# Performance work log

Measured on AMD Instinct MI355X. Metric: run time of the kernel, lower is better.

The kernel has to match this reference:

```python
import math
import jax, jax.numpy as jnp
import numpy as np

B, S, T, C, H = 4, 100, 128, 256, 256
NH, DH = 4, 32            # num_attention_heads//2, hidden_size//num_attention_heads
AH = NH * DH              # all_head_size = 128
FH = 32                   # fire_hidden_size
MAX_SP, MAX_TM, MAX_DOY = 180.0, 365.0, 182.0


def _fire(dist, c, w1, w2, max_dist):
    # FIREDistanceBias: log-compressed distance -> MLP(1->FH, SiLU, FH->1, no bias)
    c = jnp.maximum(c, 0.0)
    d = jnp.log(c * dist + 1.0) / jnp.log(c * max_dist + 1.0)
    h = jax.nn.silu(d[..., None] * w1[:, 0])   # (..., FH)
    return h @ w2[0]                            # (...,)


def setup_inputs() -> dict:
    key = jax.random.key(0)
    ks = jax.random.split(key, 20)
    p = 0.02
    inp = {
        "hidden_states": jax.random.normal(ks[0], (B, S, T, H), jnp.float32),
        "source_embeddings": jax.random.normal(ks[1], (B, S, C, H), jnp.float32),
        "attention_mask": jnp.zeros((B, 1, 1, T, C), jnp.float32),
        "st_dist": jax.random.uniform(ks[2], (B, T, C, 2), jnp.float32)
                   * jnp.array([MAX_SP, MAX_TM], jnp.float32),
        "st_doy_dist": jax.random.uniform(ks[3], (B, T, C), jnp.float32) * MAX_DOY,
        # attention projections (Linear H->AH with bias), output dense (AH->H)
        "Wq": jax.random.normal(ks[4], (AH, H), jnp.float32) * p,
        "bq": jnp.zeros((AH,), jnp.float32),
        "Wk": jax.random.normal(ks[5], (AH, H), jnp.float32) * p,
        "bk": jnp.zeros((AH,), jnp.float32),
        "Wv": jax.random.normal(ks[6], (AH, H), jnp.float32) * p,
        "bv": jnp.zeros((AH,), jnp.float32),
        "Wo": jax.random.normal(ks[7], (H, AH), jnp.float32) * p,
        "bo": jnp.zeros((H,), jnp.float32),
        # FIRE params: spatial / temporal / seasonal
        "c_s": jnp.float32(100.0),
        "w1_s": jax.random.normal(ks[8], (FH, 1), jnp.float32) * 0.5,
        "w2_s": jax.random.normal(ks[9], (1, FH), jnp.float32) * 0.5,
        "c_t": jnp.float32(100.0),
        "w1_t": jax.random.normal(ks[10], (FH, 1), jnp.float32) * 0.5,
        "w2_t": jax.random.normal(ks[11], (1, FH), jnp.float32) * 0.5,
        "c_d": jnp.float32(100.0),
        "w1_d": jax.random.normal(ks[12], (FH, 1), jnp.float32) * 0.5,
        "w2_d": jax.random.normal(ks[13], (1, FH), jnp.float32) * 0.5,
        # per-species log scales (init zeros in torch)
        "s_log_scale": jnp.zeros((S,), jnp.float32),
        "t_log_scale": jnp.zeros((S,), jnp.float32),
    }
    return inp


def reference(hidden_states, source_embeddings, attention_mask, st_dist, st_doy_dist,
              Wq, bq, Wk, bk, Wv, bv, Wo, bo,
              c_s, w1_s, w2_s, c_t, w1_t, w2_t, c_d, w1_d, w2_d,
              s_log_scale, t_log_scale):
    # FIRE distance biases over (B, T, C)
    sb = _fire(st_dist[..., 0], c_s, w1_s, w2_s, MAX_SP)
    tb = _fire(st_dist[..., 1], c_t, w1_t, w2_t, MAX_TM)
    db = _fire(st_doy_dist, c_d, w1_d, w2_d, MAX_DOY)
    # (B, S, T, C): species-scaled spatial+temporal + seasonal bias
    bias = (sb[:, None] * jnp.exp(s_log_scale)[None, :, None, None]
            + tb[:, None] * jnp.exp(t_log_scale)[None, :, None, None]
            + db[:, None])

    # projections; split heads: (B,S,L,AH) -> (B,S,NH,L,DH)
    q = (hidden_states @ Wq.T + bq).reshape(B, S, T, NH, DH).transpose(0, 1, 3, 2, 4)
    k = (source_embeddings @ Wk.T + bk).reshape(B, S, C, NH, DH).transpose(0, 1, 3, 2, 4)
    v = (source_embeddings @ Wv.T + bv).reshape(B, S, C, NH, DH).transpose(0, 1, 3, 2, 4)

    scores = jnp.einsum('bshtd,bshcd->bshtc', q, k) / math.sqrt(DH)
    scores = scores + attention_mask + bias[:, :, None]   # mask (B,1,1,T,C), bias (B,S,1,T,C)
    probs = jax.nn.softmax(scores, axis=-1)
    ctx = jnp.einsum('bshtc,bshcd->bshtd', probs, v)
    ctx = ctx.transpose(0, 1, 3, 2, 4).reshape(B, S, T, AH)
    return ctx @ Wo.T + bo   # STCrossOutput dense (dropout=0, eval)
```

## Files before the change

### kernel.cpp

```cpp
#include <hip/hip_runtime.h>
#include <hip/hip_bf16.h>
#include <math.h>

#define Bdim 4
#define Sdim 100
#define Tdim 128
#define Cdim 256
#define Hdim 256
#define NHd  4
#define DHd  32
#define AHd  128

typedef short bf16x8 __attribute__((ext_vector_type(8)));
typedef float f32x4 __attribute__((ext_vector_type(4)));

#define WAITCNT_V(n) do { \
  asm volatile("s_waitcnt vmcnt(" #n ")" ::: "memory"); \
  __builtin_amdgcn_sched_barrier(0); \
} while (0)

__device__ __forceinline__ short f2b(float x) {
  unsigned u = __float_as_uint(x);
  unsigned r = (u + 0x7FFF + ((u >> 16) & 1)) >> 16;
  return (short)r;
}

__device__ __forceinline__ void split2(float x, short& hi, short& lo) {
  unsigned u = __float_as_uint(x) & 0xFFFF0000u;
  hi = (short)(u >> 16);
  lo = f2b(x - __uint_as_float(u));
}

__device__ __forceinline__ float fire_eval(float dist, float c,
                                           const float* __restrict__ w1,
                                           const float* __restrict__ w2,
                                           float maxd) {
  c = fmaxf(c, 0.0f);
  float d = logf(fmaf(c, dist, 1.0f)) / logf(fmaf(c, maxd, 1.0f));
  float acc = 0.0f;
#pragma unroll
  for (int j = 0; j < 32; ++j) {
    float x = d * w1[j];
    float h = x / (1.0f + expf(-x));
    acc = fmaf(h, w2[j], acc);
  }
  return acc;
}

__global__ __launch_bounds__(256) void fire_bias_kernel(
    const float* __restrict__ st_dist, const float* __restrict__ st_doy,
    const float* __restrict__ mask,
    const float* __restrict__ c_s, const float* __restrict__ w1_s, const float* __restrict__ w2_s,
    const float* __restrict__ c_t, const float* __restrict__ w1_t, const float* __restrict__ w2_t,
    const float* __restrict__ c_d, const float* __restrict__ w1_d, const float* __restrict__ w2_d,
    float4* __restrict__ pk) {
  int i = blockIdx.x * 256 + threadIdx.x;
  if (i >= Bdim * Tdim * Cdim) return;
  float2 dv = ((const float2*)st_dist)[i];
  float4 r;
  r.x = fire_eval(dv.x, c_s[0], w1_s, w2_s, 180.0f);
  r.y = fire_eval(dv.y, c_t[0], w1_t, w2_t, 365.0f);
  r.z = fire_eval(st_doy[i], c_d[0], w1_d, w2_d, 182.0f) + mask[i];
  r.w = 0.0f;
  pk[i] = r;
}

__global__ __launch_bounds__(256) void bias_combine(
    const float4* __restrict__ pk,
    const float* __restrict__ sls, const float* __restrict__ tls,
    float* __restrict__ bC) {
  const int b = blockIdx.y;
  const int base = blockIdx.x * 1024 + threadIdx.x * 4;
  const float4* src = pk + (size_t)b * Tdim * Cdim + base;
  float sb[4], tb[4], db[4];
#pragma unroll
  for (int i = 0; i < 4; ++i) {
    float4 v = src[i];
    sb[i] = v.x; tb[i] = v.y; db[i] = v.z;
  }
  float* dst = bC + ((size_t)b * Sdim) * Tdim * Cdim + base;
  for (int s = 0; s < Sdim; ++s) {
    float es = __expf(sls[s]), et = __expf(tls[s]);
    float4 o;
    o.x = fmaf(sb[0], es, fmaf(tb[0], et, db[0]));
    o.y = fmaf(sb[1], es, fmaf(tb[1], et, db[1]));
    o.z = fmaf(sb[2], es, fmaf(tb[2], et, db[2]));
    o.w = fmaf(sb[3], es, fmaf(tb[3], et, db[3]));
    *(float4*)(dst + (size_t)s * Tdim * Cdim) = o;
  }
}

__global__ __launch_bounds__(256) void wsplit_pack(
    const float* __restrict__ Wq, const float* __restrict__ Wk,
    const float* __restrict__ Wv, const float* __restrict__ Wo,
    short* __restrict__ pack) {
  int which = blockIdx.y;
  const float* W = which == 0 ? Wq : which == 1 ? Wk : which == 2 ? Wv : Wo;
  int idx = blockIdx.x * 256 + threadIdx.x;
  int j = idx & 7;
  int l = (idx >> 3) & 63;
  int frag = idx >> 9;
  int nt, kk8, Kd;
  if (which == 3) { nt = frag & 15; kk8 = frag >> 4; Kd = 128; }
  else           { nt = frag & 7;  kk8 = frag >> 3; Kd = 256; }
  int n = nt * 16 + (l & 15);
  int k = kk8 * 32 + (l >> 4) * 8 + j;
  short h, lo_;
  split2(W[(size_t)n * Kd + k], h, lo_);
  pack[(size_t)which * 65536 + idx] = h;
  pack[(size_t)which * 65536 + 32768 + idx] = lo_;
}


__global__ __launch_bounds__(512, 4) void proj_q_mfma(
    const float* __restrict__ A, const short* __restrict__ Wp,
    const float* __restrict__ bias, short* __restrict__ O, float scale) {
  __shared__ short wlds[2][16 * 512];
  const int tid = threadIdx.x;
  const int l = tid & 63, w = tid >> 6;
  const int lr = l & 15, lg = l >> 4;
  const int m0 = blockIdx.x * 128;
  const int arow = m0 + w * 16 + lr;
  const float* ap = A + (size_t)arow * 256 + lg * 8;

  auto stage = [&](int buf, int kk) {
#pragma unroll
    for (int r = 0; r < 2; ++r) {
      int f = w + 8 * r;
      const short* gsrc = Wp + (r ? 32768 : 0) + ((size_t)(kk * 8 + w) * 64 + l) * 8;
      int loff = __builtin_amdgcn_readfirstlane(buf * 8192 + f * 512);
      __builtin_amdgcn_global_load_lds(gsrc, &wlds[0][0] + loff, 16, 0, 0);
    }
  };

  f32x4 acc[8] = {};
  stage(0, 0);
  float4 ca = *(const float4*)ap;
  float4 cb = *(const float4*)(ap + 4);
#pragma unroll
  for (int kk = 0; kk < 8; ++kk) {
    const int buf = kk & 1;
    float4 na, nb;
    if (kk < 7) {
      stage(buf ^ 1, kk + 1);
      const float* np = ap + (kk + 1) * 32;
      na = *(const float4*)np;
      nb = *(const float4*)(np + 4);
    }
    float av[8] = {ca.x, ca.y, ca.z, ca.w, cb.x, cb.y, cb.z, cb.w};
    bf16x8 ahi, alo;
#pragma unroll
    for (int e = 0; e < 8; ++e) { short h, lo_; split2(av[e], h, lo_); ahi[e] = h; alo[e] = lo_; }
    if (kk < 7) { WAITCNT_V(4); } else { WAITCNT_V(0); }
    __builtin_amdgcn_s_barrier();
    const short* lb = &wlds[0][0] + buf * 8192 + l * 8;
#pragma unroll
    for (int nt = 0; nt < 8; ++nt) {
      bf16x8 whi = *(const bf16x8*)(lb + nt * 512);
      bf16x8 wlo = *(const bf16x8*)(lb + (8 + nt) * 512);
      acc[nt] = __builtin_amdgcn_mfma_f32_16x16x32_bf16(ahi, whi, acc[nt], 0, 0, 0);
      acc[nt] = __builtin_amdgcn_mfma_f32_16x16x32_bf16(ahi, wlo, acc[nt], 0, 0, 0);
      acc[nt] = __builtin_amdgcn_mfma_f32_16x16x32_bf16(alo, whi, acc[nt], 0, 0, 0);
    }
    __builtin_amdgcn_s_barrier();
    if (kk < 7) { ca = na; cb = nb; }
  }
#pragma unroll
  for (int nt = 0; nt < 8; ++nt)
#pragma unroll
    for (int r = 0; r < 4; ++r)
      O[(size_t)(m0 + w * 16 + lg * 4 + r) * 128 + nt * 16 + lr] =
          f2b((acc[nt][r] + bias[nt * 16 + lr]) * scale);
}

__global__ __launch_bounds__(512, 4) void proj_kv_mfma(
    const float* __restrict__ A,
    const short* __restrict__ Wkp, const float* __restrict__ bk,
    const short* __restrict__ Wvp, const float* __restrict__ bv,
    short* __restrict__ Ko, short* __restrict__ Vo) {
  __shared__ short wlds[2][32 * 512];
  const int tid = threadIdx.x;
  const int l = tid & 63, w = tid >> 6;
  const int lr = l & 15, lg = l >> 4;
  const int m0 = blockIdx.x * 128;
  const int arow = m0 + w * 16 + lr;
  const float* ap = A + (size_t)arow * 256 + lg * 8;

  auto stage = [&](int buf, int kk) {
#pragma unroll
    for (int r = 0; r < 4; ++r) {
      int f = w + 8 * r;
      const short* gsrc = ((f >> 4) ? Wvp : Wkp) + (((f >> 3) & 1) ? 32768 : 0)
                          + ((size_t)(kk * 8 + (f & 7)) * 64 + l) * 8;
      int loff = __builtin_amdgcn_readfirstlane(buf * 16384 + f * 512);
      __builtin_amdgcn_global_load_lds(gsrc, &wlds[0][0] + loff, 16, 0, 0);
    }
  };

  f32x4 accK[8] = {}, accV[8] = {};
  stage(0, 0);
  float4 ca = *(const float4*)ap;
  float4 cb = *(const float4*)(ap + 4);
#pragma unroll
  for (int kk = 0; kk < 8; ++kk) {
    const int buf = kk & 1;
    float4 na, nb;
    if (kk < 7) {
      stage(buf ^ 1, kk + 1);
      const float* np = ap + (kk + 1) * 32;
      na = *(const float4*)np;
      nb = *(const float4*)(np + 4);
    }
    float av[8] = {ca.x, ca.y, ca.z, ca.w, cb.x, cb.y, cb.z, cb.w};
    bf16x8 ahi, alo;
#pragma unroll
    for (int e = 0; e < 8; ++e) { short h, lo_; split2(av[e], h, lo_); ahi[e] = h; alo[e] = lo_; }
    if (kk < 7) { WAITCNT_V(6); } else { WAITCNT_V(0); }
    __builtin_amdgcn_s_barrier();
    const short* lb = &wlds[0][0] + buf * 16384 + l * 8;
#pragma unroll
    for (int nt = 0; nt < 8; ++nt) {
      bf16x8 khi = *(const bf16x8*)(lb + nt * 512);
      bf16x8 klo = *(const bf16x8*)(lb + (8 + nt) * 512);
      bf16x8 vhi = *(const bf16x8*)(lb + (16 + nt) * 512);
      bf16x8 vlo = *(const bf16x8*)(lb + (24 + nt) * 512);
      accK[nt] = __builtin_amdgcn_mfma_f32_16x16x32_bf16(ahi, khi, accK[nt], 0, 0, 0);
      accK[nt] = __builtin_amdgcn_mfma_f32_16x16x32_bf16(ahi, klo, accK[nt], 0, 0, 0);
      accK[nt] = __builtin_amdgcn_mfma_f32_16x16x32_bf16(alo, khi, accK[nt], 0, 0, 0);
      accV[nt] = __builtin_amdgcn_mfma_f32_16x16x32_bf16(ahi, vhi, accV[nt], 0, 0, 0);
      accV[nt] = __builtin_amdgcn_mfma_f32_16x16x32_bf16(ahi, vlo, accV[nt], 0, 0, 0);
      accV[nt] = __builtin_amdgcn_mfma_f32_16x16x32_bf16(alo, vhi, accV[nt], 0, 0, 0);
    }
    __builtin_amdgcn_s_barrier();
    if (kk < 7) { ca = na; cb = nb; }
  }
#pragma unroll
  for (int nt = 0; nt < 8; ++nt)
#pragma unroll
    for (int r = 0; r < 4; ++r) {
      size_t row = (size_t)(m0 + w * 16 + lg * 4 + r) * 128 + nt * 16 + lr;
      Ko[row] = f2b(accK[nt][r] + bk[nt * 16 + lr]);
      Vo[row] = f2b(accV[nt][r] + bv[nt * 16 + lr]);
    }
}

__global__ __launch_bounds__(512, 4) void proj_o_mfma(
    const short* __restrict__ Ahi, const short* __restrict__ Alo,
    const short* __restrict__ Wp, const float* __restrict__ bias,
    float* __restrict__ O) {
  __shared__ short wlds[2][32 * 512];
  const int tid = threadIdx.x;
  const int l = tid & 63, w = tid >> 6;
  const int lr = l & 15, lg = l >> 4;
  const int m0 = blockIdx.x * 128;
  const int arow = m0 + w * 16 + lr;
  const short* ah = Ahi + (size_t)arow * 128 + lg * 8;
  const short* al = Alo + (size_t)arow * 128 + lg * 8;

  auto stage = [&](int buf, int kk) {
#pragma unroll
    for (int r = 0; r < 4; ++r) {
      int f = w + 8 * r;
      const short* gsrc = Wp + ((f >> 4) ? 32768 : 0)
                          + ((size_t)(kk * 16 + (f & 15)) * 64 + l) * 8;
      int loff = __builtin_amdgcn_readfirstlane(buf * 16384 + f * 512);
      __builtin_amdgcn_global_load_lds(gsrc, &wlds[0][0] + loff, 16, 0, 0);
    }
  };

  f32x4 acc[16] = {};
  stage(0, 0);
  bf16x8 cah = *(const bf16x8*)ah;
  bf16x8 cal = *(const bf16x8*)al;
#pragma unroll
  for (int kk = 0; kk < 4; ++kk) {
    const int buf = kk & 1;
    bf16x8 nah, nal;
    if (kk < 3) {
      stage(buf ^ 1, kk + 1);
      nah = *(const bf16x8*)(ah + (kk + 1) * 32);
      nal = *(const bf16x8*)(al + (kk + 1) * 32);
    }
    if (kk < 3) { WAITCNT_V(6); } else { WAITCNT_V(0); }
    __builtin_amdgcn_s_barrier();
    const short* lb = &wlds[0][0] + buf * 16384 + l * 8;
#pragma unroll
    for (int nt = 0; nt < 16; ++nt) {
      bf16x8 whi = *(const bf16x8*)(lb + nt * 512);
      bf16x8 wlo = *(const bf16x8*)(lb + (16 + nt) * 512);
      acc[nt] = __builtin_amdgcn_mfma_f32_16x16x32_bf16(cah, whi, acc[nt], 0, 0, 0);
      acc[nt] = __builtin_amdgcn_mfma_f32_16x16x32_bf16(cah, wlo, acc[nt], 0, 0, 0);
      acc[nt] = __builtin_amdgcn_mfma_f32_16x16x32_bf16(cal, whi, acc[nt], 0, 0, 0);
    }
    __builtin_amdgcn_s_barrier();
    if (kk < 3) { cah = nah; cal = nal; }
  }
#pragma unroll
  for (int nt = 0; nt < 16; ++nt)
#pragma unroll
    for (int r = 0; r < 4; ++r)
      O[(size_t)(m0 + w * 16 + lg * 4 + r) * 256 + nt * 16 + lr] =
          acc[nt][r] + bias[nt * 16 + lr];
}

__global__ __launch_bounds__(512) void attn_mfma(
    const short* __restrict__ Qb, const short* __restrict__ Kb,
    const short* __restrict__ Vb,
    const float* __restrict__ bC,
    short* __restrict__ Chi, short* __restrict__ Clo) {
  __shared__ short vfrag[8][2][64][8];
  __shared__ short pbuf[8][16 * 36];

  const int tid = threadIdx.x;
  const int l = tid & 63;
  const int w = tid >> 6;
  const int lr = l & 15, lg = l >> 4;
  const int bid = blockIdx.x;
  const int xcd = bid & 7;
  const int i_  = bid >> 3;
  const int bs  = xcd * 50 + (i_ >> 2);
  const int h   = i_ & 3;

  const size_t kvbase = (size_t)bs * Cdim * AHd + h * DHd;
  const size_t qbase  = (size_t)bs * Tdim * AHd + h * DHd;

#pragma unroll
  for (int rep = 0; rep < 2; ++rep) {
    int chunk = tid * 2 + rep;
    int c = chunk >> 2, q = chunk & 3;
    bf16x8 v8 = *(const bf16x8*)(Vb + kvbase + (size_t)c * AHd + q * 8);
    int kc = c >> 5, nt = q >> 1;
    int lanebase = ((c & 31) >> 3) * 16 + (q & 1) * 8;
    int j = c & 7;
#pragma unroll
    for (int e = 0; e < 8; ++e)
      vfrag[kc][nt][lanebase + e][j] = v8[e];
  }
  __syncthreads();

  bf16x8 qf = *(const bf16x8*)(Qb + qbase + (size_t)(w * 16 + lr) * AHd + lg * 8);
  bf16x8 kf[16];
#pragma unroll
  for (int nt = 0; nt < 16; ++nt)
    kf[nt] = *(const bf16x8*)(Kb + kvbase + (size_t)(nt * 16 + lr) * AHd + lg * 8);

  const float* bb = bC + (size_t)bs * Tdim * Cdim + (size_t)(w * 16) * Cdim;
  f32x4 sacc[16];
#pragma unroll
  for (int nt = 0; nt < 16; ++nt) {
    f32x4 cinit;
#pragma unroll
    for (int r = 0; r < 4; ++r)
      cinit[r] = bb[(size_t)(lg * 4 + r) * Cdim + nt * 16 + lr];
    sacc[nt] = __builtin_amdgcn_mfma_f32_16x16x32_bf16(qf, kf[nt], cinit, 0, 0, 0);
  }

  float rinv[4];
#pragma unroll
  for (int nt = 0; nt < 16; ++nt)
#pragma unroll
    for (int r = 0; r < 4; ++r)
      sacc[nt][r] = __expf(sacc[nt][r]);
#pragma unroll
  for (int r = 0; r < 4; ++r) {
    float su = 0.f;
#pragma unroll
    for (int nt = 0; nt < 16; ++nt) su += sacc[nt][r];
#pragma unroll
    for (int off = 1; off < 16; off <<= 1) su += __shfl_xor(su, off);
    rinv[r] = 1.0f / su;
  }

  const f32x4 zero = {0.f, 0.f, 0.f, 0.f};
  f32x4 cacc[2] = {zero, zero};
  short* pb = &pbuf[w][0];
#pragma unroll
  for (int kc = 0; kc < 8; ++kc) {
#pragma unroll
    for (int ntl = 0; ntl < 2; ++ntl) {
      int nt = kc * 2 + ntl;
#pragma unroll
      for (int r = 0; r < 4; ++r)
        pb[(lg * 4 + r) * 36 + ntl * 16 + lr] = f2b(sacc[nt][r]);
    }
    bf16x8 af = *(const bf16x8*)&pb[lr * 36 + lg * 8];
#pragma unroll
    for (int ntd = 0; ntd < 2; ++ntd) {
      bf16x8 vf = *(const bf16x8*)&vfrag[kc][ntd][l][0];
      cacc[ntd] = __builtin_amdgcn_mfma_f32_16x16x32_bf16(af, vf, cacc[ntd], 0, 0, 0);
    }
  }

#pragma unroll
  for (int ntd = 0; ntd < 2; ++ntd)
#pragma unroll
    for (int r = 0; r < 4; ++r) {
      float val = cacc[ntd][r] * rinv[r];
      short h_, lo_;
      split2(val, h_, lo_);
      size_t idx = qbase + (size_t)(w * 16 + lg * 4 + r) * AHd + ntd * 16 + lr;
      Chi[idx] = h_;
      Clo[idx] = lo_;
    }
}

extern "C" void kernel_launch(void* const* d_in, const int* in_sizes, int n_in,
                              void* d_out, int out_size, void* d_ws, size_t ws_size,
                              hipStream_t stream) {
  const float* hs     = (const float*)d_in[0];
  const float* se     = (const float*)d_in[1];
  const float* mask   = (const float*)d_in[2];
  const float* stdist = (const float*)d_in[3];
  const float* stdoy  = (const float*)d_in[4];
  const float* Wq = (const float*)d_in[5];
  const float* bq = (const float*)d_in[6];
  const float* Wk = (const float*)d_in[7];
  const float* bk = (const float*)d_in[8];
  const float* Wv = (const float*)d_in[9];
  const float* bv = (const float*)d_in[10];
  const float* Wo = (const float*)d_in[11];
  const float* bo = (const float*)d_in[12];
  const float* c_s  = (const float*)d_in[13];
  const float* w1_s = (const float*)d_in[14];
  const float* w2_s = (const float*)d_in[15];
  const float* c_t  = (const float*)d_in[16];
  const float* w1_t = (const float*)d_in[17];
  const float* w2_t = (const float*)d_in[18];
  const float* c_d  = (const float*)d_in[19];
  const float* w1_d = (const float*)d_in[20];
  const float* w2_d = (const float*)d_in[21];
  const float* sls  = (const float*)d_in[22];
  const float* tls  = (const float*)d_in[23];
  float* out = (float*)d_out;

  float* ws = (float*)d_ws;
  const size_t BTC  = (size_t)Bdim * Tdim * Cdim;
  const size_t BSTC = (size_t)Bdim * Sdim * Tdim * Cdim;
  const size_t NQ   = (size_t)Bdim * Sdim * Tdim * AHd;
  const size_t NKV  = (size_t)Bdim * Sdim * Cdim * AHd;

  float4* pk  = (float4*)ws;
  float* bC   = ws + 4 * BTC;
  short* wpck = (short*)(bC + BSTC);
  short* Qb   = wpck + 262144;
  short* Kb   = Qb + NQ;
  short* Vb   = Kb + NKV;
  short* Chi  = Vb + NKV;
  short* Clo  = Chi + NQ;

  const int MQ  = Bdim * Sdim * Tdim;
  const int MKV = Bdim * Sdim * Cdim;

  fire_bias_kernel<<<(Bdim * Tdim * Cdim + 255) / 256, 256, 0, stream>>>(
      stdist, stdoy, mask, c_s, w1_s, w2_s, c_t, w1_t, w2_t, c_d, w1_d, w2_d, pk);

  bias_combine<<<dim3(Tdim * Cdim / 1024, Bdim), 256, 0, stream>>>(pk, sls, tls, bC);

  wsplit_pack<<<dim3(128, 4), 256, 0, stream>>>(Wq, Wk, Wv, Wo, wpck);

  proj_q_mfma<<<dim3(MQ / 128), 512, 0, stream>>>(hs, wpck, bq, Qb,
                                                  0.17677669529663687f);
  proj_kv_mfma<<<dim3(MKV / 128), 512, 0, stream>>>(
      se, wpck + 65536, bk, wpck + 131072, bv, Kb, Vb);

  attn_mfma<<<dim3(Bdim * Sdim * NHd), 512, 0, stream>>>(
      Qb, Kb, Vb, bC, Chi, Clo);

  proj_o_mfma<<<dim3(MQ / 128), 512, 0, stream>>>(Chi, Clo, wpck + 196608, bo, out);
}
```

Before: 183.2 us.

## Retile projection GEMMs so each wave covers two M tiles and half N

The Q, KV and output projection kernels now give each wave two 16-row M tiles and half of the N columns, instead of one M tile across all N. Each LDS weight fragment read then feeds twice as many MFMAs, halving LDS read traffic per MFMA. In exchange every row of A is loaded by two waves, which doubles global/L2 reads of the activation operand and duplicates the fp32-to-bf16 split work. The wait counts are adjusted for the extra in-flight loads.

```diff
diff --git a/kernel.cpp b/kernel.cpp
--- a/kernel.cpp
+++ b/kernel.cpp
@@ -119,9 +119,10 @@
   const int tid = threadIdx.x;
   const int l = tid & 63, w = tid >> 6;
   const int lr = l & 15, lg = l >> 4;
+  const int g = w >> 2, q = w & 3;
   const int m0 = blockIdx.x * 128;
-  const int arow = m0 + w * 16 + lr;
-  const float* ap = A + (size_t)arow * 256 + lg * 8;
+  const float* ap0 = A + (size_t)(m0 + q * 32 + lr) * 256 + lg * 8;
+  const float* ap1 = ap0 + (size_t)16 * 256;
 
   auto stage = [&](int buf, int kk) {
 #pragma unroll
@@ -133,44 +134,63 @@
     }
   };
 
-  f32x4 acc[8] = {};
+  f32x4 acc[2][4] = {};
   stage(0, 0);
-  float4 ca = *(const float4*)ap;
-  float4 cb = *(const float4*)(ap + 4);
+  float4 c0a = *(const float4*)ap0;
+  float4 c0b = *(const float4*)(ap0 + 4);
+  float4 c1a = *(const float4*)ap1;
+  float4 c1b = *(const float4*)(ap1 + 4);
 #pragma unroll
   for (int kk = 0; kk < 8; ++kk) {
     const int buf = kk & 1;
-    float4 na, nb;
+    bf16x8 ahi[2], alo[2];
+    {
+      float av0[8] = {c0a.x, c0a.y, c0a.z, c0a.w, c0b.x, c0b.y, c0b.z, c0b.w};
+      float av1[8] = {c1a.x, c1a.y, c1a.z, c1a.w, c1b.x, c1b.y, c1b.z, c1b.w};
+#pragma unroll
+      for (int e = 0; e < 8; ++e) {
+        short h, lo_;
+        split2(av0[e], h, lo_); ahi[0][e] = h; alo[0][e] = lo_;
+        split2(av1[e], h, lo_); ahi[1][e] = h; alo[1][e] = lo_;
+      }
+    }
     if (kk < 7) {
       stage(buf ^ 1, kk + 1);
-      const float* np = ap + (kk + 1) * 32;
-      na = *(const float4*)np;
-      nb = *(const float4*)(np + 4);
-    }
-    float av[8] = {ca.x, ca.y, ca.z, ca.w, cb.x, cb.y, cb.z, cb.w};
-    bf16x8 ahi, alo;
-#pragma unroll
-    for (int e = 0; e < 8; ++e) { short h, lo_; split2(av[e], h, lo_); ahi[e] = h; alo[e] = lo_; }
-    if (kk < 7) { WAITCNT_V(4); } else { WAITCNT_V(0); }
+      const int nk = (kk + 1) * 32;
+      c0a = *(const float4*)(ap0 + nk);
+      c0b = *(const float4*)(ap0 + nk + 4);
+      c1a = *(const float4*)(ap1 + nk);
+      c1b = *(const float4*)(ap1 + nk + 4);
+      WAITCNT_V(6);
+    } else {
+      WAITCNT_V(0);
+    }
     __builtin_amdgcn_s_barrier();
     const short* lb = &wlds[0][0] + buf * 8192 + l * 8;
 #pragma unroll
-    for (int nt = 0; nt < 8; ++nt) {
-      bf16x8 whi = *(const bf16x8*)(lb + nt * 512);
-      bf16x8 wlo = *(const bf16x8*)(lb + (8 + nt) * 512);
-      acc[nt] = __builtin_amdgcn_mfma_f32_16x16x32_bf16(ahi, whi, acc[nt], 0, 0, 0);
-      acc[nt] = __builtin_amdgcn_mfma_f32_16x16x32_bf16(ahi, wlo, acc[nt], 0, 0, 0);
-      acc[nt] = __builtin_amdgcn_mfma_f32_16x16x32_bf16(alo, whi, acc[nt], 0, 0, 0);
+    for (int nt = 0; nt < 4; ++nt) {
+      const int ntp = g * 4 + nt;
+      bf16x8 whi = *(const bf16x8*)(lb + ntp * 512);
+      bf16x8 wlo = *(const bf16x8*)(lb + (8 + ntp) * 512);
+#pragma unroll
+      for (int mi = 0; mi < 2; ++mi) {
+        acc[mi][nt] = __builtin_amdgcn_mfma_f32_16x16x32_bf16(ahi[mi], whi, acc[mi][nt], 0, 0, 0);
+        acc[mi][nt] = __builtin_amdgcn_mfma_f32_16x16x32_bf16(ahi[mi], wlo, acc[mi][nt], 0, 0, 0);
+        acc[mi][nt] = __builtin_amdgcn_mfma_f32_16x16x32_bf16(alo[mi], whi, acc[mi][nt], 0, 0, 0);
+      }
     }
     __builtin_amdgcn_s_barrier();
-    if (kk < 7) { ca = na; cb = nb; }
-  }
-#pragma unroll
-  for (int nt = 0; nt < 8; ++nt)
-#pragma unroll
-    for (int r = 0; r < 4; ++r)
-      O[(size_t)(m0 + w * 16 + lg * 4 + r) * 128 + nt * 16 + lr] =
-          f2b((acc[nt][r] + bias[nt * 16 + lr]) * scale);
+  }
+#pragma unroll
+  for (int mi = 0; mi < 2; ++mi)
+#pragma unroll
+    for (int nt = 0; nt < 4; ++nt)
+#pragma unroll
+      for (int r = 0; r < 4; ++r) {
+        int col = (g * 4 + nt) * 16 + lr;
+        O[(size_t)(m0 + q * 32 + mi * 16 + lg * 4 + r) * 128 + col] =
+            f2b((acc[mi][nt][r] + bias[col]) * scale);
+      }
 }
 
 __global__ __launch_bounds__(512, 4) void proj_kv_mfma(
@@ -182,9 +202,10 @@
   const int tid = threadIdx.x;
   const int l = tid & 63, w = tid >> 6;
   const int lr = l & 15, lg = l >> 4;
+  const int half = w >> 2, q = w & 3;
   const int m0 = blockIdx.x * 128;
-  const int arow = m0 + w * 16 + lr;
-  const float* ap = A + (size_t)arow * 256 + lg * 8;
+  const float* ap0 = A + (size_t)(m0 + q * 32 + lr) * 256 + lg * 8;
+  const float* ap1 = ap0 + (size_t)16 * 256;
 
   auto stage = [&](int buf, int kk) {
 #pragma unroll
@@ -197,51 +218,63 @@
     }
   };
 
-  f32x4 accK[8] = {}, accV[8] = {};
+  f32x4 acc[2][8] = {};
   stage(0, 0);
-  float4 ca = *(const float4*)ap;
-  float4 cb = *(const float4*)(ap + 4);
+  float4 c0a = *(const float4*)ap0;
+  float4 c0b = *(const float4*)(ap0 + 4);
+  float4 c1a = *(const float4*)ap1;
+  float4 c1b = *(const float4*)(ap1 + 4);
 #pragma unroll
   for (int kk = 0; kk < 8; ++kk) {
     const int buf = kk & 1;
-    float4 na, nb;
+    bf16x8 ahi[2], alo[2];
+    {
+      float av0[8] = {c0a.x, c0a.y, c0a.z, c0a.w, c0b.x, c0b.y, c0b.z, c0b.w};
+      float av1[8] = {c1a.x, c1a.y, c1a.z, c1a.w, c1b.x, c1b.y, c1b.z, c1b.w};
+#pragma unroll
+      for (int e = 0; e < 8; ++e) {
+        short h, lo_;
+        split2(av0[e], h, lo_); ahi[0][e] = h; alo[0][e] = lo_;
+        split2(av1[e], h, lo_); ahi[1][e] = h; alo[1][e] = lo_;
+      }
+    }
     if (kk < 7) {
       stage(buf ^ 1, kk + 1);
-      const float* np = ap + (kk + 1) * 32;
-      na = *(const float4*)np;
-      nb = *(const float4*)(np + 4);
-    }
-    float av[8] = {ca.x, ca.y, ca.z, ca.w, cb.x, cb.y, cb.z, cb.w};
-    bf16x8 ahi, alo;
-#pragma unroll
-    for (int e = 0; e < 8; ++e) { short h, lo_; split2(av[e], h, lo_); ahi[e] = h; alo[e] = lo_; }
-    if (kk < 7) { WAITCNT_V(6); } else { WAITCNT_V(0); }
+      const int nk = (kk + 1) * 32;
+      c0a = *(const float4*)(ap0 + nk);
+      c0b = *(const float4*)(ap0 + nk + 4);
+      c1a = *(const float4*)(ap1 + nk);
+      c1b = *(const float4*)(ap1 + nk + 4);
+      WAITCNT_V(8);
+    } else {
+      WAITCNT_V(0);
+    }
     __builtin_amdgcn_s_barrier();
-    const short* lb = &wlds[0][0] + buf * 16384 + l * 8;
+    const short* lb = &wlds[0][0] + buf * 16384 + half * 16 * 512 + l * 8;
 #pragma unroll
     for (int nt = 0; nt < 8; ++nt) {
-      bf16x8 khi = *(const bf16x8*)(lb + nt * 512);
-      bf16x8 klo = *(const bf16x8*)(lb + (8 + nt) * 512);
-      bf16x8 vhi = *(const bf16x8*)(lb + (16 + nt) * 512);
-      bf16x8 vlo = *(const bf16x8*)(lb + (24 + nt) * 512);
-      accK[nt] = __builtin_amdgcn_mfma_f32_16x16x32_bf16(ahi, khi, accK[nt], 0, 0, 0);
-      accK[nt] = __builtin_amdgcn_mfma_f32_16x16x32_bf16(ahi, klo, accK[nt], 0, 0, 0);
-      accK[nt] = __builtin_amdgcn_mfma_f32_16x16x32_bf16(alo, khi, accK[nt], 0, 0, 0);
-      accV[nt] = __builtin_amdgcn_mfma_f32_16x16x32_bf16(ahi, vhi, accV[nt], 0, 0, 0);
-      accV[nt] = __builtin_amdgcn_mfma_f32_16x16x32_bf16(ahi, vlo, accV[nt], 0, 0, 0);
-      accV[nt] = __builtin_amdgcn_mfma_f32_16x16x32_bf16(alo, vhi, accV[nt], 0, 0, 0);
+      bf16x8 whi = *(const bf16x8*)(lb + nt * 512);
+      bf16x8 wlo = *(const bf16x8*)(lb + (8 + nt) * 512);
+#pragma unroll
+      for (int mi = 0; mi < 2; ++mi) {
+        acc[mi][nt] = __builtin_amdgcn_mfma_f32_16x16x32_bf16(ahi[mi], whi, acc[mi][nt], 0, 0, 0);
+        acc[mi][nt] = __builtin_amdgcn_mfma_f32_16x16x32_bf16(ahi[mi], wlo, acc[mi][nt], 0, 0, 0);
+        acc[mi][nt] = __builtin_amdgcn_mfma_f32_16x16x32_bf16(alo[mi], whi, acc[mi][nt], 0, 0, 0);
+      }
     }
     __builtin_amdgcn_s_barrier();
-    if (kk < 7) { ca = na; cb = nb; }
-  }
-#pragma unroll
-  for (int nt = 0; nt < 8; ++nt)
-#pragma unroll
-    for (int r = 0; r < 4; ++r) {
-      size_t row = (size_t)(m0 + w * 16 + lg * 4 + r) * 128 + nt * 16 + lr;
-      Ko[row] = f2b(accK[nt][r] + bk[nt * 16 + lr]);
-      Vo[row] = f2b(accV[nt][r] + bv[nt * 16 + lr]);
-    }
+  }
+  short* __restrict__ O = half ? Vo : Ko;
+  const float* __restrict__ bias = half ? bv : bk;
+#pragma unroll
+  for (int mi = 0; mi < 2; ++mi)
+#pragma unroll
+    for (int nt = 0; nt < 8; ++nt)
+#pragma unroll
+      for (int r = 0; r < 4; ++r) {
+        size_t row = (size_t)(m0 + q * 32 + mi * 16 + lg * 4 + r) * 128 + nt * 16 + lr;
+        O[row] = f2b(acc[mi][nt][r] + bias[nt * 16 + lr]);
+      }
 }
 
 __global__ __launch_bounds__(512, 4) void proj_o_mfma(
@@ -252,10 +285,12 @@
   const int tid = threadIdx.x;
   const int l = tid & 63, w = tid >> 6;
   const int lr = l & 15, lg = l >> 4;
+  const int g = w >> 2, q = w & 3;
   const int m0 = blockIdx.x * 128;
-  const int arow = m0 + w * 16 + lr;
-  const short* ah = Ahi + (size_t)arow * 128 + lg * 8;
-  const short* al = Alo + (size_t)arow * 128 + lg * 8;
+  const short* ah0 = Ahi + (size_t)(m0 + q * 32 + lr) * 128 + lg * 8;
+  const short* al0 = Alo + (size_t)(m0 + q * 32 + lr) * 128 + lg * 8;
+  const short* ah1 = ah0 + (size_t)16 * 128;
+  const short* al1 = al0 + (size_t)16 * 128;
 
   auto stage = [&](int buf, int kk) {
 #pragma unroll
@@ -268,39 +303,54 @@
     }
   };
 
-  f32x4 acc[16] = {};
+  f32x4 acc[2][8] = {};
   stage(0, 0);
-  bf16x8 cah = *(const bf16x8*)ah;
-  bf16x8 cal = *(const bf16x8*)al;
+  bf16x8 cah0 = *(const bf16x8*)ah0;
+  bf16x8 cal0 = *(const bf16x8*)al0;
+  bf16x8 cah1 = *(const bf16x8*)ah1;
+  bf16x8 cal1 = *(const bf16x8*)al1;
 #pragma unroll
   for (int kk = 0; kk < 4; ++kk) {
     const int buf = kk & 1;
-    bf16x8 nah, nal;
+    bf16x8 ahi[2] = {cah0, cah1};
+    bf16x8 alo[2] = {cal0, cal1};
     if (kk < 3) {
       stage(buf ^ 1, kk + 1);
-      nah = *(const bf16x8*)(ah + (kk + 1) * 32);
-      nal = *(const bf16x8*)(al + (kk + 1) * 32);
-    }
-    if (kk < 3) { WAITCNT_V(6); } else { WAITCNT_V(0); }
+      const int nk = (kk + 1) * 32;
+      cah0 = *(const bf16x8*)(ah0 + nk);
+      cal0 = *(const bf16x8*)(al0 + nk);
+      cah1 = *(const bf16x8*)(ah1 + nk);
+      cal1 = *(const bf16x8*)(al1 + nk);
+      WAITCNT_V(8);
+    } else {
+      WAITCNT_V(0);
+    }
     __builtin_amdgcn_s_barrier();
     const short* lb = &wlds[0][0] + buf * 16384 + l * 8;
 #pragma unroll
-    for (int nt = 0; nt < 16; ++nt) {
-      bf16x8 whi = *(const bf16x8*)(lb + nt * 512);
-      bf16x8 wlo = *(const bf16x8*)(lb + (16 + nt) * 512);
-      acc[nt] = __builtin_amdgcn_mfma_f32_16x16x32_bf16(cah, whi, acc[nt], 0, 0, 0);
-      acc[nt] = __builtin_amdgcn_mfma_f32_16x16x32_bf16(cah, wlo, acc[nt], 0, 0, 0);
-      acc[nt] = __builtin_amdgcn_mfma_f32_16x16x32_bf16(cal, whi, acc[nt], 0, 0, 0);
+    for (int nt = 0; nt < 8; ++nt) {
+      const int ntp = g * 8 + nt;
+      bf16x8 whi = *(const bf16x8*)(lb + ntp * 512);
+      bf16x8 wlo = *(const bf16x8*)(lb + (16 + ntp) * 512);
+#pragma unroll
+      for (int mi = 0; mi < 2; ++mi) {
+        acc[mi][nt] = __builtin_amdgcn_mfma_f32_16x16x32_bf16(ahi[mi], whi, acc[mi][nt], 0, 0, 0);
+        acc[mi][nt] = __builtin_amdgcn_mfma_f32_16x16x32_bf16(ahi[mi], wlo, acc[mi][nt], 0, 0, 0);
+        acc[mi][nt] = __builtin_amdgcn_mfma_f32_16x16x32_bf16(alo[mi], whi, acc[mi][nt], 0, 0, 0);
+      }
     }
     __builtin_amdgcn_s_barrier();
-    if (kk < 3) { cah = nah; cal = nal; }
-  }
-#pragma unroll
-  for (int nt = 0; nt < 16; ++nt)
-#pragma unroll
-    for (int r = 0; r < 4; ++r)
-      O[(size_t)(m0 + w * 16 + lg * 4 + r) * 256 + nt * 16 + lr] =
-          acc[nt][r] + bias[nt * 16 + lr];
+  }
+#pragma unroll
+  for (int mi = 0; mi < 2; ++mi)
+#pragma unroll
+    for (int nt = 0; nt < 8; ++nt)
+#pragma unroll
+      for (int r = 0; r < 4; ++r) {
+        int col = (g * 8 + nt) * 16 + lr;
+        O[(size_t)(m0 + q * 32 + mi * 16 + lg * 4 + r) * 256 + col] =
+            acc[mi][nt][r] + bias[col];
+      }
 }
 
 __global__ __launch_bounds__(512) void attn_mfma(
```

Result: slower. 291.5 us (+59.1%).
